# Kernel optimization log

Measured on AMD Instinct MI355X. Metric: run time of the kernel, lower is better.

The kernel has to match this reference:

```python
import jax, jax.numpy as jnp
import numpy as np

B = 32768
N_PATCH = 196  # 14x14 grid of 2x2 patches over a 28x28 image
DIM = 16       # 2^4 state-vector dimension for 4 wires


def setup_inputs() -> dict:
    key = jax.random.key(0)
    kx, = jax.random.split(key, 1)
    # pixel data in [0,1] like normalized MNIST
    x = jax.random.uniform(kx, (B, 784), dtype=jnp.float32)
    # fixed random 2-qubit layer composed into a single real orthogonal 16x16 unitary
    rng = np.random.default_rng(0)
    q, _ = np.linalg.qr(rng.standard_normal((DIM, DIM)))
    U = jnp.asarray(q, dtype=jnp.float32)
    return {"x": x, "U": U}


def _pauli_z_signs():
    # Z[w, b] = +1 if bit w of basis index b is 0 else -1 (wire 0 = MSB, kron order)
    wires = jnp.arange(4)[:, None]
    basis = jnp.arange(DIM)[None, :]
    bits = (basis >> (3 - wires)) & 1
    return 1.0 - 2.0 * bits.astype(jnp.float32)  # [4, 16]


def reference(x, U):
    bsz = x.shape[0]
    img = x.reshape(bsz, 28, 28)
    # extract 2x2 patches in the same row-major order as the original loop:
    # data = [x[r,c], x[r,c+1], x[r+1,c], x[r+1,c+1]] -> [B, 196, 4]
    data = img.reshape(bsz, 14, 2, 14, 2).transpose(0, 1, 3, 2, 4).reshape(bsz, N_PATCH, 4)
    # RY(theta)|0> = cos(theta/2)|0> + sin(theta/2)|1> per wire (real amplitudes)
    half = 0.5 * data
    q = jnp.stack([jnp.cos(half), jnp.sin(half)], axis=-1)  # [B, 196, 4, 2]
    # product state via kron over the 4 wires -> [B, 196, 16]
    state = jnp.einsum('bpi,bpj,bpk,bpl->bpijkl',
                       q[:, :, 0], q[:, :, 1], q[:, :, 2], q[:, :, 3]
                       ).reshape(bsz, N_PATCH, DIM)
    # apply the fixed random layer unitary
    state = jnp.einsum('bpd,ed->bpe', state, U)
    # PauliZ expectation on each wire from |amp|^2
    probs = state * state
    Z = _pauli_z_signs()  # [4, 16]
    meas = jnp.einsum('bpd,wd->bpw', probs, Z)  # [B, 196, 4]
    return meas.reshape(bsz, N_PATCH * 4)
```

## Files before the change

kernel.cpp:

```cpp
#include <hip/hip_runtime.h>

typedef _Float16 half4 __attribute__((ext_vector_type(4)));
typedef _Float16 h2 __attribute__((ext_vector_type(2)));
typedef float f32x4 __attribute__((ext_vector_type(4)));

#define SINCONST 0.07957747154594767f

__device__ __forceinline__ unsigned int pk(float a, float b) {
    return __builtin_bit_cast(unsigned int, __builtin_amdgcn_cvt_pkrtz(a, b));
}

__device__ __forceinline__ void factors(float px0, float px1, float px2, float px3,
                                        uint4& ad, uint2& qd) {
    float t0 = px0 * SINCONST, t1 = px1 * SINCONST;
    float t2 = px2 * SINCONST, t3 = px3 * SINCONST;
    float s0 = __builtin_amdgcn_sinf(t0), c0 = __builtin_amdgcn_cosf(t0);
    float s1 = __builtin_amdgcn_sinf(t1), c1 = __builtin_amdgcn_cosf(t1);
    float s2 = __builtin_amdgcn_sinf(t2), c2 = __builtin_amdgcn_cosf(t2);
    float s3 = __builtin_amdgcn_sinf(t3), c3 = __builtin_amdgcn_cosf(t3);
    float a0 = c0 * c1, a1 = c0 * s1, a2 = s0 * c1, a3 = s0 * s1;
    float q0 = c2 * c3, q1 = c2 * s3, q2 = s2 * c3, q3 = s2 * s3;
    ad.x = pk(a0, a0); ad.y = pk(a1, a1); ad.z = pk(a2, a2); ad.w = pk(a3, a3);
    qd.x = pk(q0, q1); qd.y = pk(q2, q3);
}

__global__ __launch_bounds__(256) void quanv(
    const float* __restrict__ x,
    const float* __restrict__ U,
    float* __restrict__ out,
    int total, int ipw, int rem)
{
    __shared__ __align__(16) unsigned int smem[4 * 768];

    const int tid  = threadIdx.x;
    const int lane = tid & 63;
    const int wib  = tid >> 6;
    const int wave = (blockIdx.x * 256 + tid) >> 6;
    const int p16  = lane & 15;
    const int g    = lane >> 4;

    unsigned int* buf = smem + wib * 768;

    half4 aU;
    {
        const float* up = U + p16 * 16 + 4 * g;
        aU[0] = (_Float16)up[0];
        aU[1] = (_Float16)up[1];
        aU[2] = (_Float16)up[2];
        aU[3] = (_Float16)up[3];
    }
    half4 aS;
    {
        int w = p16 & 3;
        #pragma unroll
        for (int i = 0; i < 4; ++i) {
            int e = 4 * g + i;
            aS[i] = ((e >> (3 - w)) & 1) ? (_Float16)-1.f : (_Float16)1.f;
        }
    }

    int cnt = ipw + (wave < rem ? 1 : 0);
    if (cnt <= 0) return;
    const int mac0 = wave * ipw + (wave < rem ? wave : rem);
    const int nPairs = total >> 1;

    auto ldp = [&](int j, float4& t4, float4& b4) {
        int PR = (mac0 + j) * 64 + lane;
        if (PR >= nPairs) PR = nPairs - 1;
        int P   = PR * 2;
        int img = P / 196;
        int pp  = P - img * 196;
        int r   = (pp * 2341) >> 15;
        const float4* ptr = reinterpret_cast<const float4*>(x + img * 784 + 2 * pp + 28 * r);
        t4 = ptr[0];
        b4 = ptr[7];
    };

    float4 cT, cB, nT, nB;
    ldp(0, cT, cB);
    ldp(1, nT, nB);

    for (int j = 0; j < cnt; ++j) {
        float4 fT, fB;
        ldp(j + 2, fT, fB);

        uint4 adA, adB; uint2 qdA, qdB;
        factors(cT.x, cT.y, cB.x, cB.y, adA, qdA);
        factors(cT.z, cT.w, cB.z, cB.w, adB, qdB);

        *reinterpret_cast<uint4*>(buf + 8 * lane)     = adA;
        *reinterpret_cast<uint4*>(buf + 8 * lane + 4) = adB;
        uint4 qq = make_uint4(qdA.x, qdA.y, qdB.x, qdB.y);
        *reinterpret_cast<uint4*>(buf + 512 + 4 * lane) = qq;

        const int pbase = (mac0 + j) * 128;
        #pragma unroll
        for (int t = 0; t < 8; ++t) {
            const int pt = t * 16 + p16;
            unsigned int adw = buf[pt * 4 + g];
            uint2 qw = *reinterpret_cast<const uint2*>(buf + 512 + 2 * pt);

            h2 ag  = __builtin_bit_cast(h2, adw);
            h2 q01 = __builtin_bit_cast(h2, qw.x);
            h2 q23 = __builtin_bit_cast(h2, qw.y);
            h2 blo = ag * q01;
            h2 bhi = ag * q23;
            half4 bST = __builtin_shufflevector(blo, bhi, 0, 1, 2, 3);

            const f32x4 zero4 = {0.f, 0.f, 0.f, 0.f};
            f32x4 y = __builtin_amdgcn_mfma_f32_16x16x16f16(aU, bST, zero4, 0, 0, 0);

            h2 y01 = __builtin_bit_cast(h2, pk(y[0], y[1]));
            h2 y23 = __builtin_bit_cast(h2, pk(y[2], y[3]));
            h2 p01 = y01 * y01;
            h2 p23 = y23 * y23;
            half4 bP = __builtin_shufflevector(p01, p23, 0, 1, 2, 3);

            f32x4 m = __builtin_amdgcn_mfma_f32_16x16x16f16(aS, bP, zero4, 0, 0, 0);

            int Ps = pbase + pt;
            if (g == 0 && Ps < total) {
                __builtin_nontemporal_store(m, reinterpret_cast<f32x4*>(out + (size_t)Ps * 4));
            }
        }

        cT = nT; cB = nB;
        nT = fT; nB = fB;
    }
}

extern "C" void kernel_launch(void* const* d_in, const int* in_sizes, int n_in,
                              void* d_out, int out_size, void* d_ws, size_t ws_size,
                              hipStream_t stream) {
    const float* x = (const float*)d_in[0];
    const float* U = (const float*)d_in[1];
    float* out = (float*)d_out;

    int B = in_sizes[0] / 784;
    int total = B * 196;
    int nPairs = total / 2;
    int nmac = (nPairs + 63) / 64;

    int nblocks = 1792;
    int nwaves = nblocks * (256 / 64);
    int ipw = nmac / nwaves;
    int rem = nmac % nwaves;

    quanv<<<nblocks, 256, 0, stream>>>(x, U, out, total, ipw, rem);
}
```

Baseline: 41.70 us.

## Double-buffer LDS factors, compact layout, and use full-wave coalesced output stores

Splits the per-pair factor buffer in LDS into two halves, so that the factors for the next macro-iteration are computed and written while the current one is consumed by the MFMAs. The A factors are stored packed and un-duplicated, halving that part of the LDS, and are duplicated in registers on load. Output stores now select among four MFMA results so that all 64 lanes write in one store rather than a quarter of the lanes writing each time. It also adds a launch-bounds occupancy hint of 7 and enlarges LDS per wave, which may raise register pressure or limit occupancy.

```diff
diff --git a/kernel.cpp b/kernel.cpp
--- a/kernel.cpp
+++ b/kernel.cpp
@@ -11,7 +11,7 @@
 }
 
 __device__ __forceinline__ void factors(float px0, float px1, float px2, float px3,
-                                        uint4& ad, uint2& qd) {
+                                        uint2& aw, uint2& qw) {
     float t0 = px0 * SINCONST, t1 = px1 * SINCONST;
     float t2 = px2 * SINCONST, t3 = px3 * SINCONST;
     float s0 = __builtin_amdgcn_sinf(t0), c0 = __builtin_amdgcn_cosf(t0);
@@ -20,17 +20,17 @@
     float s3 = __builtin_amdgcn_sinf(t3), c3 = __builtin_amdgcn_cosf(t3);
     float a0 = c0 * c1, a1 = c0 * s1, a2 = s0 * c1, a3 = s0 * s1;
     float q0 = c2 * c3, q1 = c2 * s3, q2 = s2 * c3, q3 = s2 * s3;
-    ad.x = pk(a0, a0); ad.y = pk(a1, a1); ad.z = pk(a2, a2); ad.w = pk(a3, a3);
-    qd.x = pk(q0, q1); qd.y = pk(q2, q3);
+    aw.x = pk(a0, a1); aw.y = pk(a2, a3);
+    qw.x = pk(q0, q1); qw.y = pk(q2, q3);
 }
 
-__global__ __launch_bounds__(256) void quanv(
+__global__ __launch_bounds__(256, 7) void quanv(
     const float* __restrict__ x,
     const float* __restrict__ U,
     float* __restrict__ out,
     int total, int ipw, int rem)
 {
-    __shared__ __align__(16) unsigned int smem[4 * 768];
+    __shared__ __align__(16) unsigned int smem[4 * 1024];
 
     const int tid  = threadIdx.x;
     const int lane = tid & 63;
@@ -39,7 +39,7 @@
     const int p16  = lane & 15;
     const int g    = lane >> 4;
 
-    unsigned int* buf = smem + wib * 768;
+    unsigned int* wbase = smem + wib * 1024;
 
     half4 aU;
     {
@@ -76,56 +76,66 @@
         b4 = ptr[7];
     };
 
-    float4 cT, cB, nT, nB;
+    auto do_factors = [&](int jj, float4 T, float4 Bt) {
+        unsigned int* buf = wbase + (jj & 1) * 512;
+        uint2 awA, qwA, awB, qwB;
+        factors(T.x, T.y, Bt.x, Bt.y, awA, qwA);
+        factors(T.z, T.w, Bt.z, Bt.w, awB, qwB);
+        *reinterpret_cast<uint4*>(buf + lane * 4)       = make_uint4(awA.x, awA.y, awB.x, awB.y);
+        *reinterpret_cast<uint4*>(buf + 256 + lane * 4) = make_uint4(qwA.x, qwA.y, qwB.x, qwB.y);
+    };
+
+    float4 cT, cB, fT, fB;
     ldp(0, cT, cB);
-    ldp(1, nT, nB);
+    ldp(1, fT, fB);
+    do_factors(0, cT, cB);
 
     for (int j = 0; j < cnt; ++j) {
-        float4 fT, fB;
+        cT = fT; cB = fB;
         ldp(j + 2, fT, fB);
 
-        uint4 adA, adB; uint2 qdA, qdB;
-        factors(cT.x, cT.y, cB.x, cB.y, adA, qdA);
-        factors(cT.z, cT.w, cB.z, cB.w, adB, qdB);
+        do_factors(j + 1, cT, cB);
 
-        *reinterpret_cast<uint4*>(buf + 8 * lane)     = adA;
-        *reinterpret_cast<uint4*>(buf + 8 * lane + 4) = adB;
-        uint4 qq = make_uint4(qdA.x, qdA.y, qdB.x, qdB.y);
-        *reinterpret_cast<uint4*>(buf + 512 + 4 * lane) = qq;
+        const unsigned int* buf2 = wbase + (j & 1) * 512;
+        const unsigned short* ap = reinterpret_cast<const unsigned short*>(buf2);
+        const int pbase = (mac0 + j) * 128;
 
-        const int pbase = (mac0 + j) * 128;
         #pragma unroll
-        for (int t = 0; t < 8; ++t) {
-            const int pt = t * 16 + p16;
-            unsigned int adw = buf[pt * 4 + g];
-            uint2 qw = *reinterpret_cast<const uint2*>(buf + 512 + 2 * pt);
+        for (int th = 0; th < 2; ++th) {
+            f32x4 mm[4];
+            #pragma unroll
+            for (int i = 0; i < 4; ++i) {
+                const int t  = th * 4 + i;
+                const int pt = t * 16 + p16;
+                unsigned int av = ap[pt * 4 + g];
+                unsigned int dup = (av << 16) | av;
+                uint2 qw = *reinterpret_cast<const uint2*>(buf2 + 256 + pt * 2);
 
-            h2 ag  = __builtin_bit_cast(h2, adw);
-            h2 q01 = __builtin_bit_cast(h2, qw.x);
-            h2 q23 = __builtin_bit_cast(h2, qw.y);
-            h2 blo = ag * q01;
-            h2 bhi = ag * q23;
-            half4 bST = __builtin_shufflevector(blo, bhi, 0, 1, 2, 3);
+                h2 ag  = __builtin_bit_cast(h2, dup);
+                h2 q01 = __builtin_bit_cast(h2, qw.x);
+                h2 q23 = __builtin_bit_cast(h2, qw.y);
+                h2 blo = ag * q01;
+                h2 bhi = ag * q23;
+                half4 bST = __builtin_shufflevector(blo, bhi, 0, 1, 2, 3);
 
-            const f32x4 zero4 = {0.f, 0.f, 0.f, 0.f};
-            f32x4 y = __builtin_amdgcn_mfma_f32_16x16x16f16(aU, bST, zero4, 0, 0, 0);
+                const f32x4 zero4 = {0.f, 0.f, 0.f, 0.f};
+                f32x4 y = __builtin_amdgcn_mfma_f32_16x16x16f16(aU, bST, zero4, 0, 0, 0);
 
-            h2 y01 = __builtin_bit_cast(h2, pk(y[0], y[1]));
-            h2 y23 = __builtin_bit_cast(h2, pk(y[2], y[3]));
-            h2 p01 = y01 * y01;
-            h2 p23 = y23 * y23;
-            half4 bP = __builtin_shufflevector(p01, p23, 0, 1, 2, 3);
+                h2 y01 = __builtin_bit_cast(h2, pk(y[0], y[1]));
+                h2 y23 = __builtin_bit_cast(h2, pk(y[2], y[3]));
+                h2 p01 = y01 * y01;
+                h2 p23 = y23 * y23;
+                half4 bP = __builtin_shufflevector(p01, p23, 0, 1, 2, 3);
 
-            f32x4 m = __builtin_amdgcn_mfma_f32_16x16x16f16(aS, bP, zero4, 0, 0, 0);
-
-            int Ps = pbase + pt;
-            if (g == 0 && Ps < total) {
-                __builtin_nontemporal_store(m, reinterpret_cast<f32x4*>(out + (size_t)Ps * 4));
+                mm[i] = __builtin_amdgcn_mfma_f32_16x16x16f16(aS, bP, zero4, 0, 0, 0);
             }
+            f32x4 sa  = (g & 1) ? mm[1] : mm[0];
+            f32x4 sb  = (g & 1) ? mm[3] : mm[2];
+            f32x4 sel = (g & 2) ? sb : sa;
+            int Ps = pbase + th * 64 + lane;
+            if (Ps < total)
+                __builtin_nontemporal_store(sel, reinterpret_cast<f32x4*>(out + (size_t)Ps * 4));
         }
-
-        cT = nT; cB = nB;
-        nT = fT; nB = fB;
     }
 }
 
```

After: 41.00 us. About the same (-1.7%).
